# Performance work log

Measured on AMD Instinct MI355X. Metric: run time of the kernel, lower is better.

## Reference

```python
import jax, jax.numpy as jnp
import numpy as np

N_FREQS = 6  # PositionEmbedding default used by LISA


def setup_inputs() -> dict:
    key = jax.random.key(0)
    ks = jax.random.split(key, 8)
    B, L, N, D, H = 8, 32768, 2048, 64, 256
    in_dim = 1 * (2 * N_FREQS + 1) + 3 * D  # 13 + 192 = 205

    def w(k, i, o):
        return jax.random.normal(k, (i, o), jnp.float32) * (1.0 / np.sqrt(i))

    return {
        "coord": jax.random.uniform(ks[0], (B, L, 1), jnp.float32),
        "latent": jax.random.normal(ks[1], (B, N, D), jnp.float32),
        "W0": w(ks[2], in_dim, H), "b0": jnp.zeros((H,), jnp.float32),
        "W1": w(ks[3], H, H), "b1": jnp.zeros((H,), jnp.float32),
        "W2": w(ks[4], H, H), "b2": jnp.zeros((H,), jnp.float32),
        "W3": w(ks[5], H, H), "b3": jnp.zeros((H,), jnp.float32),
        "W4": w(ks[6], H, 1), "b4": jnp.zeros((1,), jnp.float32),
    }


def reference(coord, latent, W0, b0, W1, b1, W2, b2, W3, b3, W4, b4):
    B, N, D = latent.shape
    # feat_unfold: concat shifted-prev / self / shifted-next along channels
    feat = jnp.swapaxes(latent, 1, 2)                                   # [B, D, N]
    feat_prev = jnp.concatenate([feat[:, :, :1], feat[:, :, :-1]], axis=2)
    feat_next = jnp.concatenate([feat[:, :, 1:], feat[:, :, -1:]], axis=2)
    feat = jnp.concatenate([feat_prev, feat, feat_next], axis=1)        # [B, 3D, N]

    # grid_sample(bilinear, padding_mode='border', align_corners=False) on a
    # 1-row image: y coordinate 0 hits row 0 exactly, so only x interpolates.
    # torch mapping: ix = ((gx + 1) * W - 1) / 2 with gx = coord*2 - 1
    ix = coord[..., 0] * N - 0.5                                        # [B, L]
    x0 = jnp.floor(ix)
    t = ix - x0                                                         # lerp weight
    i0 = jnp.clip(x0.astype(jnp.int32), 0, N - 1)                       # border clamp
    i1 = jnp.clip(x0.astype(jnp.int32) + 1, 0, N - 1)
    f0 = jnp.take_along_axis(feat, i0[:, None, :], axis=2)              # [B, 3D, L]
    f1 = jnp.take_along_axis(feat, i1[:, None, :], axis=2)
    sampled = (1.0 - t)[:, None, :] * f0 + t[:, None, :] * f1
    sampled = jnp.swapaxes(sampled, 1, 2)                               # [B, L, 3D]

    # positional encoding: [x, sin(f x), cos(f x) for f in 1,2,4,8,16,32]
    freqs = 2.0 ** jnp.arange(N_FREQS, dtype=jnp.float32)
    ang = coord * freqs                                                 # [B, L, 6]
    pe = jnp.stack([jnp.sin(ang), jnp.cos(ang)], axis=-1)
    pe = pe.reshape(ang.shape[0], ang.shape[1], 2 * N_FREQS)            # [B, L, 12]

    inp = jnp.concatenate([coord, pe, sampled], axis=-1)                # [B, L, 205]

    h = jax.nn.relu(inp @ W0 + b0)
    h = jax.nn.relu(h @ W1 + b1)
    h = jax.nn.relu(h @ W2 + b2)
    h = jax.nn.relu(h @ W3 + b3)
    return h @ W4 + b4                                                  # [B, L, 1]
```

## Files before the change

kernel.cpp:

```cpp
#include <hip/hip_runtime.h>
#include <hip/hip_bf16.h>

typedef unsigned short ushort_t;
typedef unsigned int uint_t;
typedef __attribute__((ext_vector_type(8))) short short8;
typedef __attribute__((ext_vector_type(4))) float float4v;
typedef __attribute__((ext_vector_type(4))) uint_t uint4v;

#define NLAT 2048
#define DLAT 64

#define PW_BASE 128
#define PW0_OFF 0
#define PW1_OFF 57344
#define PW2_OFF 122880
#define PW3_OFF 188416

__device__ __forceinline__ float b2f(ushort_t u) {
  union { uint_t i; float f; } v; v.i = ((uint_t)u) << 16; return v.f;
}
__device__ __forceinline__ ushort_t f2b(float f) {
  uint_t x = __float_as_uint(f);
  uint_t r = (x + 0x7fffu + ((x >> 16) & 1u)) >> 16;
  return (ushort_t)r;
}
__device__ __forceinline__ uint_t pack2(float lo, float hi) {
  float2 t; t.x = lo; t.y = hi;
  union { __hip_bfloat162 h; uint_t u; } cv;
  cv.h = __float22bfloat162_rn(t);
  return cv.u;
}
__device__ __forceinline__ int imin(int a, int b) { return a < b ? a : b; }
__device__ __forceinline__ int imax(int a, int b) { return a > b ? a : b; }

__device__ __forceinline__ float ldv(const float* p, long i)    { return p[i]; }
__device__ __forceinline__ float ldv(const ushort_t* p, long i) { return b2f(p[i]); }
__device__ __forceinline__ void stv(float* p, long i, float v)    { p[i] = v; }
__device__ __forceinline__ void stv(ushort_t* p, long i, float v) { p[i] = f2b(v); }

__device__ __forceinline__ float4 load4f(const float* p) { return *(const float4*)p; }
__device__ __forceinline__ float4 load4f(const ushort_t* p) {
  uint2 u = *(const uint2*)p;
  float4 r;
  r.x = b2f((ushort_t)(u.x & 0xffffu)); r.y = b2f((ushort_t)(u.x >> 16));
  r.z = b2f((ushort_t)(u.y & 0xffffu)); r.w = b2f((ushort_t)(u.y >> 16));
  return r;
}

__device__ __forceinline__ void async_copy16(const ushort_t* g, ushort_t* l) {
  __builtin_amdgcn_global_load_lds(
      (const __attribute__((address_space(1))) void*)g,
      (__attribute__((address_space(3))) void*)l, 16, 0, 0);
}

__device__ __forceinline__ void stage_q(int gi, ushort_t* dst,
                                        const ushort_t* __restrict__ pw, int tid) {
  int layer = gi >> 2, q = gi & 3;
  int KT = (layer == 0) ? 7 : 8;
  int loff = (layer == 0) ? PW0_OFF : (layer == 1) ? PW1_OFF
           : (layer == 2) ? PW2_OFF : PW3_OFF;
  const ushort_t* src = pw + loff + q * KT * 2048;
  int n = KT * 256;
  for (int i = tid; i < n; i += 256)
    async_copy16(src + (size_t)i * 8, dst + (size_t)i * 8);
}

__global__ void detect_mode(const ushort_t* __restrict__ lat, int* __restrict__ flag) {
  if (threadIdx.x == 0) *flag = 0;
  __syncthreads();
  int big = 0;
  for (int i = threadIdx.x; i < 1024; i += 64) {
    float v = b2f(lat[i]);
    if (!(fabsf(v) < 1e5f)) big = 1;
  }
  if (__any(big) && threadIdx.x == 0) *flag = 1;
}

template <typename TI>
__global__ void pack_w_t(const TI* __restrict__ W0, const TI* __restrict__ W1,
                         const TI* __restrict__ W2, const TI* __restrict__ W3,
                         ushort_t* __restrict__ pw, const int* __restrict__ flag, int want)
{
  if (*flag != want) return;
  int g = blockIdx.x * blockDim.x + threadIdx.x;
  if (g >= 31 * 1024) return;
  int lane = g & 63, q = lane >> 4;
  int mt   = (g >> 6) & 15;
  int ktg  = g >> 10;
  const TI* W; ushort_t* dst; int kt, KT; bool isw0 = false;
  if (ktg < 7)       { W = W0; dst = pw + PW0_OFF; kt = ktg;      KT = 7; isw0 = true; }
  else if (ktg < 15) { W = W1; dst = pw + PW1_OFF; kt = ktg - 7;  KT = 8; }
  else if (ktg < 23) { W = W2; dst = pw + PW2_OFF; kt = ktg - 15; KT = 8; }
  else               { W = W3; dst = pw + PW3_OFF; kt = ktg - 23; KT = 8; }
  int col = mt * 16 + (lane & 15);
  uint_t words[4];
#pragma unroll
  for (int h = 0; h < 4; ++h) {
    ushort_t vv[2];
#pragma unroll
    for (int e = 0; e < 2; ++e) {
      int j = 2 * h + e;
      int f = 32 * kt + 16 * (j >> 2) + 4 * q + (j & 3);
      int row = f;
      if (isw0) row = (f < 192) ? (13 + f) : (f == 192 ? 0 : (f <= 204 ? f - 192 : -1));
      vv[e] = (row >= 0) ? f2b(ldv(W, (long)row * 256 + col)) : (ushort_t)0;
    }
    words[h] = (uint_t)vv[0] | ((uint_t)vv[1] << 16);
  }
  uint4 o; o.x = words[0]; o.y = words[1]; o.z = words[2]; o.w = words[3];
  *(uint4*)(dst + ((size_t)(mt * KT + kt) * 64 + lane) * 8) = o;
}

template <int KT>
__device__ __forceinline__ void run_layer(int base, float4v (&acc)[16][2],
                                          const uint4v (&hu)[8][2],
                                          ushort_t (*wbuf)[16384],
                                          const ushort_t* __restrict__ pw,
                                          int tid, int lane)
{
#pragma unroll
  for (int qq = 0; qq < 4; ++qq) {
    const int gi = base + qq;
    if (gi + 1 < 16) stage_q(gi + 1, wbuf[(gi + 1) & 1], pw, tid);
    const ushort_t* buf = wbuf[gi & 1];
#pragma unroll
    for (int m = 0; m < 4; ++m) {
      acc[qq * 4 + m][0] = (float4v){0.f, 0.f, 0.f, 0.f};
      acc[qq * 4 + m][1] = (float4v){0.f, 0.f, 0.f, 0.f};
    }
#pragma unroll
    for (int kt = 0; kt < KT; ++kt) {
      short8 b0 = __builtin_bit_cast(short8, hu[kt][0]);
      short8 b1 = __builtin_bit_cast(short8, hu[kt][1]);
#pragma unroll
      for (int m = 0; m < 4; ++m) {
        short8 a = *(const short8*)&buf[((size_t)(m * KT + kt) * 64 + lane) * 8];
        acc[qq * 4 + m][0] = __builtin_amdgcn_mfma_f32_16x16x32_bf16(a, b0, acc[qq * 4 + m][0], 0, 0, 0);
        acc[qq * 4 + m][1] = __builtin_amdgcn_mfma_f32_16x16x32_bf16(a, b1, acc[qq * 4 + m][1], 0, 0, 0);
      }
    }
    __syncthreads();
  }
}

__device__ __forceinline__ void convert_layer(float4v (&acc)[16][2], uint4v (&hu)[8][2],
                                              const float* bwl, int q)
{
#pragma unroll
  for (int mt = 0; mt < 16; ++mt) {
    float4 b4 = *(const float4*)&bwl[mt * 16 + 4 * q];
#pragma unroll
    for (int g = 0; g < 2; ++g) {
      float v0 = fmaxf(acc[mt][g][0] + b4.x, 0.f);
      float v1 = fmaxf(acc[mt][g][1] + b4.y, 0.f);
      float v2 = fmaxf(acc[mt][g][2] + b4.z, 0.f);
      float v3 = fmaxf(acc[mt][g][3] + b4.w, 0.f);
      hu[mt >> 1][g][(mt & 1) * 2 + 0] = pack2(v0, v1);
      hu[mt >> 1][g][(mt & 1) * 2 + 1] = pack2(v2, v3);
    }
  }
}

template <typename TI>
__global__ __launch_bounds__(256, 2) void lisa_fused_t(
    const TI* __restrict__ coord, const TI* __restrict__ latent,
    const TI* __restrict__ bias0, const TI* __restrict__ bias1,
    const TI* __restrict__ bias2, const TI* __restrict__ bias3,
    const TI* __restrict__ W4,    const TI* __restrict__ b4,
    const ushort_t* __restrict__ pw, TI* __restrict__ out,
    const int* __restrict__ flag, int want)
{
  if (*flag != want) return;
  __shared__ __align__(16) ushort_t wbuf[2][16384];
  __shared__ __align__(16) float bw[4 * 256 + 256 + 1];

  const int tid  = threadIdx.x;
  const int lane = tid & 63, q = lane >> 4, m15 = lane & 15;
  const int wv   = tid >> 6;
  const long pbase = (long)blockIdx.x * 128 + wv * 32 + m15;

  stage_q(0, wbuf[0], pw, tid);
  for (int i = tid; i < 1281; i += 256) {
    float v;
    if (i < 256)       v = ldv(bias0, i);
    else if (i < 512)  v = ldv(bias1, i - 256);
    else if (i < 768)  v = ldv(bias2, i - 512);
    else if (i < 1024) v = ldv(bias3, i - 768);
    else if (i < 1280) v = ldv(W4, i - 1024);
    else               v = ldv(b4, 0);
    bw[i] = v;
  }

  uint4v hu[8][2];
#pragma unroll
  for (int g = 0; g < 2; ++g) {
    long p = pbase + g * 16;
    float c   = ldv(coord, p);
    float ixv = c * 2048.0f - 0.5f;
    float x0f = floorf(ixv);
    float t   = ixv - x0f;
    int   x0  = (int)x0f;
    int   i0  = imin(imax(x0, 0), NLAT - 1);
    int   i1  = imin(imax(x0 + 1, 0), NLAT - 1);
    float w0 = 1.0f - t, w1 = t;
    int rows0[3] = { imax(i0 - 1, 0), i0, imin(i0 + 1, NLAT - 1) };
    int rows1[3] = { imax(i1 - 1, 0), i1, imin(i1 + 1, NLAT - 1) };
    const TI* lat = latent + (size_t)(p >> 15) * (NLAT * DLAT);
#pragma unroll
    for (int tb = 0; tb < 12; ++tb) {
      int region = tb >> 2;
      int d0 = 16 * (tb & 3) + 4 * q;
      float4 a = load4f(lat + (long)rows0[region] * DLAT + d0);
      float4 b = load4f(lat + (long)rows1[region] * DLAT + d0);
      hu[tb >> 1][g][(tb & 1) * 2 + 0] = pack2(w0 * a.x + w1 * b.x, w0 * a.y + w1 * b.y);
      hu[tb >> 1][g][(tb & 1) * 2 + 1] = pack2(w0 * a.z + w1 * b.z, w0 * a.w + w1 * b.w);
    }
    float pv[4];
#pragma unroll
    for (int s = 0; s < 4; ++s) {
      int f = 192 + 4 * q + s;
      float v = 0.0f;
      if (f == 192) v = c;
      else if (f <= 204) {
        int i = f - 193;
        float fr = (float)(1 << (i >> 1));
        float ang = c * fr;
        v = (i & 1) ? __cosf(ang) : __sinf(ang);
      }
      pv[s] = v;
    }
    hu[6][g][0] = pack2(pv[0], pv[1]);
    hu[6][g][1] = pack2(pv[2], pv[3]);
    hu[6][g][2] = 0; hu[6][g][3] = 0;
  }
  __syncthreads();

  float4v acc[16][2];

  run_layer<7>( 0, acc, hu, wbuf, pw, tid, lane);
  convert_layer(acc, hu, bw + 0 * 256, q);
  run_layer<8>( 4, acc, hu, wbuf, pw, tid, lane);
  convert_layer(acc, hu, bw + 1 * 256, q);
  run_layer<8>( 8, acc, hu, wbuf, pw, tid, lane);
  convert_layer(acc, hu, bw + 2 * 256, q);
  run_layer<8>(12, acc, hu, wbuf, pw, tid, lane);

  float partial0 = 0.f, partial1 = 0.f;
#pragma unroll
  for (int mt = 0; mt < 16; ++mt) {
    float4 b3v = *(const float4*)&bw[3 * 256 + mt * 16 + 4 * q];
    float4 w4v = *(const float4*)&bw[1024 + mt * 16 + 4 * q];
    float v;
    v = fmaxf(acc[mt][0][0] + b3v.x, 0.f); partial0 += v * w4v.x;
    v = fmaxf(acc[mt][0][1] + b3v.y, 0.f); partial0 += v * w4v.y;
    v = fmaxf(acc[mt][0][2] + b3v.z, 0.f); partial0 += v * w4v.z;
    v = fmaxf(acc[mt][0][3] + b3v.w, 0.f); partial0 += v * w4v.w;
    v = fmaxf(acc[mt][1][0] + b3v.x, 0.f); partial1 += v * w4v.x;
    v = fmaxf(acc[mt][1][1] + b3v.y, 0.f); partial1 += v * w4v.y;
    v = fmaxf(acc[mt][1][2] + b3v.z, 0.f); partial1 += v * w4v.z;
    v = fmaxf(acc[mt][1][3] + b3v.w, 0.f); partial1 += v * w4v.w;
  }
  partial0 += __shfl_xor(partial0, 16, 64);
  partial0 += __shfl_xor(partial0, 32, 64);
  partial1 += __shfl_xor(partial1, 16, 64);
  partial1 += __shfl_xor(partial1, 32, 64);
  if (lane < 16) {
    float bb = bw[1280];
    stv(out, pbase,      partial0 + bb);
    stv(out, pbase + 16, partial1 + bb);
  }
}

extern "C" void kernel_launch(void* const* d_in, const int* in_sizes, int n_in,
                              void* d_out, int out_size, void* d_ws, size_t ws_size,
                              hipStream_t stream) {
  int* flag = (int*)d_ws;
  ushort_t* pw = (ushort_t*)d_ws + PW_BASE;

  detect_mode<<<1, 64, 0, stream>>>((const ushort_t*)d_in[1], flag);

  pack_w_t<float><<<62, 512, 0, stream>>>(
      (const float*)d_in[2], (const float*)d_in[4], (const float*)d_in[6],
      (const float*)d_in[8], pw, flag, 1);
  lisa_fused_t<float><<<2048, 256, 0, stream>>>(
      (const float*)d_in[0], (const float*)d_in[1],
      (const float*)d_in[3], (const float*)d_in[5], (const float*)d_in[7],
      (const float*)d_in[9], (const float*)d_in[10], (const float*)d_in[11],
      pw, (float*)d_out, flag, 1);

  pack_w_t<ushort_t><<<62, 512, 0, stream>>>(
      (const ushort_t*)d_in[2], (const ushort_t*)d_in[4], (const ushort_t*)d_in[6],
      (const ushort_t*)d_in[8], pw, flag, 0);
  lisa_fused_t<ushort_t><<<2048, 256, 0, stream>>>(
      (const ushort_t*)d_in[0], (const ushort_t*)d_in[1],
      (const ushort_t*)d_in[3], (const ushort_t*)d_in[5], (const ushort_t*)d_in[7],
      (const ushort_t*)d_in[9], (const ushort_t*)d_in[10], (const ushort_t*)d_in[11],
      pw, (ushort_t*)d_out, flag, 0);
}
```

Measured before the change: 236.7 us.

## Switch MLP matmuls from 16x16x32 to 32x32x16 MFMA with repacked weights

Replaces the 16x16x32 bf16 MFMA tiling with 32x32x16 MFMA, so each wave handles 32 points as one B operand. The packed weight layout, K-row permutation for the activation handoff, embedding/gather layout and final reduction are all rewritten to match. The aim is fewer MFMA instructions and LDS reads per FLOP, and a lookahead load of the A fragment to overlap LDS reads with MFMA. It risks higher register pressure from the 16-float accumulators and depends on the new K-permutation being correct.

```diff
diff --git a/kernel.cpp b/kernel.cpp
--- a/kernel.cpp
+++ b/kernel.cpp
@@ -5,6 +5,7 @@
 typedef unsigned int uint_t;
 typedef __attribute__((ext_vector_type(8))) short short8;
 typedef __attribute__((ext_vector_type(4))) float float4v;
+typedef __attribute__((ext_vector_type(16))) float float16v;
 typedef __attribute__((ext_vector_type(4))) uint_t uint4v;
 
 #define NLAT 2048
@@ -12,9 +13,9 @@
 
 #define PW_BASE 128
 #define PW0_OFF 0
-#define PW1_OFF 57344
-#define PW2_OFF 122880
-#define PW3_OFF 188416
+#define PW1_OFF 53248
+#define PW2_OFF 118784
+#define PW3_OFF 184320
 
 __device__ __forceinline__ float b2f(ushort_t u) {
   union { uint_t i; float f; } v; v.i = ((uint_t)u) << 16; return v.f;
@@ -53,14 +54,15 @@
       (__attribute__((address_space(3))) void*)l, 16, 0, 0);
 }
 
-__device__ __forceinline__ void stage_q(int gi, ushort_t* dst,
-                                        const ushort_t* __restrict__ pw, int tid) {
-  int layer = gi >> 2, q = gi & 3;
-  int KT = (layer == 0) ? 7 : 8;
-  int loff = (layer == 0) ? PW0_OFF : (layer == 1) ? PW1_OFF
-           : (layer == 2) ? PW2_OFF : PW3_OFF;
-  const ushort_t* src = pw + loff + q * KT * 2048;
-  int n = KT * 256;
+__device__ __forceinline__ void stage_gi(int gi, ushort_t* dst,
+                                         const ushort_t* __restrict__ pw, int tid) {
+  int layer = gi >> 2, qq = gi & 3;
+  const ushort_t* src; int n;
+  if (layer == 0) { src = pw + PW0_OFF + (size_t)qq * 13312; n = 1664; }
+  else {
+    int loff = (layer == 1) ? PW1_OFF : (layer == 2) ? PW2_OFF : PW3_OFF;
+    src = pw + loff + (size_t)qq * 16384; n = 2048;
+  }
   for (int i = tid; i < n; i += 256)
     async_copy16(src + (size_t)i * 8, dst + (size_t)i * 8);
 }
@@ -83,80 +85,91 @@
 {
   if (*flag != want) return;
   int g = blockIdx.x * blockDim.x + threadIdx.x;
-  if (g >= 31 * 1024) return;
-  int lane = g & 63, q = lane >> 4;
-  int mt   = (g >> 6) & 15;
-  int ktg  = g >> 10;
-  const TI* W; ushort_t* dst; int kt, KT; bool isw0 = false;
-  if (ktg < 7)       { W = W0; dst = pw + PW0_OFF; kt = ktg;      KT = 7; isw0 = true; }
-  else if (ktg < 15) { W = W1; dst = pw + PW1_OFF; kt = ktg - 7;  KT = 8; }
-  else if (ktg < 23) { W = W2; dst = pw + PW2_OFF; kt = ktg - 15; KT = 8; }
-  else               { W = W3; dst = pw + PW3_OFF; kt = ktg - 23; KT = 8; }
-  int col = mt * 16 + (lane & 15);
+  if (g >= 488 * 64) return;
+  int lane = g & 63, h = lane >> 5;
+  int fid  = g >> 6;
+  const TI* W; ushort_t* dst; int mt, kt, KTL, layer;
+  if (fid < 104) { layer = 0; W = W0; dst = pw + PW0_OFF; mt = fid / 13; kt = fid % 13; KTL = 13; }
+  else {
+    int f2 = fid - 104;
+    layer = 1 + f2 / 128;
+    int r = f2 & 127; mt = r >> 4; kt = r & 15; KTL = 16;
+    W = (layer == 1) ? W1 : (layer == 2) ? W2 : W3;
+    dst = pw + ((layer == 1) ? PW1_OFF : (layer == 2) ? PW2_OFF : PW3_OFF);
+  }
+  int col = mt * 32 + (lane & 31);
   uint_t words[4];
 #pragma unroll
-  for (int h = 0; h < 4; ++h) {
+  for (int hw = 0; hw < 4; ++hw) {
     ushort_t vv[2];
 #pragma unroll
     for (int e = 0; e < 2; ++e) {
-      int j = 2 * h + e;
-      int f = 32 * kt + 16 * (j >> 2) + 4 * q + (j & 3);
-      int row = f;
-      if (isw0) row = (f < 192) ? (13 + f) : (f == 192 ? 0 : (f <= 204 ? f - 192 : -1));
+      int j = 2 * hw + e;
+      int k = 16 * kt + 8 * h + j;
+      int row;
+      if (layer == 0) {
+        row = (k < 192) ? (13 + k) : (k == 192 ? 0 : (k <= 204 ? k - 192 : -1));
+      } else {
+        int blk = k >> 5, kl = k & 31;
+        int t = (kl >> 4) & 1, h2 = (kl >> 3) & 1, u = (kl >> 2) & 1, b = kl & 3;
+        row = 32 * blk + 8 * (2 * t + u) + 4 * h2 + b;
+      }
       vv[e] = (row >= 0) ? f2b(ldv(W, (long)row * 256 + col)) : (ushort_t)0;
     }
-    words[h] = (uint_t)vv[0] | ((uint_t)vv[1] << 16);
+    words[hw] = (uint_t)vv[0] | ((uint_t)vv[1] << 16);
   }
   uint4 o; o.x = words[0]; o.y = words[1]; o.z = words[2]; o.w = words[3];
-  *(uint4*)(dst + ((size_t)(mt * KT + kt) * 64 + lane) * 8) = o;
-}
-
-template <int KT>
-__device__ __forceinline__ void run_layer(int base, float4v (&acc)[16][2],
-                                          const uint4v (&hu)[8][2],
+  *(uint4*)(dst + ((size_t)(mt * KTL + kt) * 64 + lane) * 8) = o;
+}
+
+template <int KT, int BASE>
+__device__ __forceinline__ void run_layer(float16v (&acc)[8],
+                                          const uint4v (&hu)[16],
                                           ushort_t (*wbuf)[16384],
                                           const ushort_t* __restrict__ pw,
                                           int tid, int lane)
 {
 #pragma unroll
   for (int qq = 0; qq < 4; ++qq) {
-    const int gi = base + qq;
-    if (gi + 1 < 16) stage_q(gi + 1, wbuf[(gi + 1) & 1], pw, tid);
+    constexpr int KTC = KT;
+    const int gi = BASE + qq;
+    if (gi + 1 < 16) stage_gi(gi + 1, wbuf[(gi + 1) & 1], pw, tid);
     const ushort_t* buf = wbuf[gi & 1];
-#pragma unroll
-    for (int m = 0; m < 4; ++m) {
-      acc[qq * 4 + m][0] = (float4v){0.f, 0.f, 0.f, 0.f};
-      acc[qq * 4 + m][1] = (float4v){0.f, 0.f, 0.f, 0.f};
-    }
-#pragma unroll
-    for (int kt = 0; kt < KT; ++kt) {
-      short8 b0 = __builtin_bit_cast(short8, hu[kt][0]);
-      short8 b1 = __builtin_bit_cast(short8, hu[kt][1]);
-#pragma unroll
-      for (int m = 0; m < 4; ++m) {
-        short8 a = *(const short8*)&buf[((size_t)(m * KT + kt) * 64 + lane) * 8];
-        acc[qq * 4 + m][0] = __builtin_amdgcn_mfma_f32_16x16x32_bf16(a, b0, acc[qq * 4 + m][0], 0, 0, 0);
-        acc[qq * 4 + m][1] = __builtin_amdgcn_mfma_f32_16x16x32_bf16(a, b1, acc[qq * 4 + m][1], 0, 0, 0);
+    float16v c0, c1;
+#pragma unroll
+    for (int i = 0; i < 16; ++i) { c0[i] = 0.f; c1[i] = 0.f; }
+    short8 aL, aH;
+    aL = *(const short8*)&buf[((size_t)(0 * KTC + 0) * 64 + lane) * 8];
+#pragma unroll
+    for (int kt = 0; kt < KTC; ++kt) {
+      aH = *(const short8*)&buf[((size_t)(1 * KTC + kt) * 64 + lane) * 8];
+      short8 b = __builtin_bit_cast(short8, hu[kt]);
+      c0 = __builtin_amdgcn_mfma_f32_32x32x16_bf16(aL, b, c0, 0, 0, 0);
+      if (kt + 1 < KTC)
+        aL = *(const short8*)&buf[((size_t)(0 * KTC + kt + 1) * 64 + lane) * 8];
+      c1 = __builtin_amdgcn_mfma_f32_32x32x16_bf16(aH, b, c1, 0, 0, 0);
+    }
+    acc[2 * qq]     = c0;
+    acc[2 * qq + 1] = c1;
+    __syncthreads();
+  }
+}
+
+__device__ __forceinline__ void convert_layer(float16v (&acc)[8], uint4v (&hu)[16],
+                                              const float* bwl, int h)
+{
+#pragma unroll
+  for (int mt = 0; mt < 8; ++mt) {
+#pragma unroll
+    for (int a = 0; a < 4; ++a) {
+      float4 bv = *(const float4*)&bwl[32 * mt + 8 * a + 4 * h];
+#pragma unroll
+      for (int b2 = 0; b2 < 2; ++b2) {
+        int rr = 4 * a + 2 * b2;
+        float v0 = fmaxf(acc[mt][rr]     + ((const float*)&bv)[2 * b2],     0.f);
+        float v1 = fmaxf(acc[mt][rr + 1] + ((const float*)&bv)[2 * b2 + 1], 0.f);
+        hu[2 * mt + (rr >> 3)][(rr & 7) >> 1] = pack2(v0, v1);
       }
-    }
-    __syncthreads();
-  }
-}
-
-__device__ __forceinline__ void convert_layer(float4v (&acc)[16][2], uint4v (&hu)[8][2],
-                                              const float* bwl, int q)
-{
-#pragma unroll
-  for (int mt = 0; mt < 16; ++mt) {
-    float4 b4 = *(const float4*)&bwl[mt * 16 + 4 * q];
-#pragma unroll
-    for (int g = 0; g < 2; ++g) {
-      float v0 = fmaxf(acc[mt][g][0] + b4.x, 0.f);
-      float v1 = fmaxf(acc[mt][g][1] + b4.y, 0.f);
-      float v2 = fmaxf(acc[mt][g][2] + b4.z, 0.f);
-      float v3 = fmaxf(acc[mt][g][3] + b4.w, 0.f);
-      hu[mt >> 1][g][(mt & 1) * 2 + 0] = pack2(v0, v1);
-      hu[mt >> 1][g][(mt & 1) * 2 + 1] = pack2(v2, v3);
     }
   }
 }
@@ -175,11 +188,11 @@
   __shared__ __align__(16) float bw[4 * 256 + 256 + 1];
 
   const int tid  = threadIdx.x;
-  const int lane = tid & 63, q = lane >> 4, m15 = lane & 15;
+  const int lane = tid & 63, h = lane >> 5, n32 = lane & 31;
   const int wv   = tid >> 6;
-  const long pbase = (long)blockIdx.x * 128 + wv * 32 + m15;
-
-  stage_q(0, wbuf[0], pw, tid);
+  const long p   = (long)blockIdx.x * 128 + wv * 32 + n32;
+
+  stage_gi(0, wbuf[0], pw, tid);
   for (int i = tid; i < 1281; i += 256) {
     float v;
     if (i < 256)       v = ldv(bias0, i);
@@ -191,10 +204,8 @@
     bw[i] = v;
   }
 
-  uint4v hu[8][2];
-#pragma unroll
-  for (int g = 0; g < 2; ++g) {
-    long p = pbase + g * 16;
+  uint4v hu[16];
+  {
     float c   = ldv(coord, p);
     float ixv = c * 2048.0f - 0.5f;
     float x0f = floorf(ixv);
@@ -207,18 +218,22 @@
     int rows1[3] = { imax(i1 - 1, 0), i1, imin(i1 + 1, NLAT - 1) };
     const TI* lat = latent + (size_t)(p >> 15) * (NLAT * DLAT);
 #pragma unroll
-    for (int tb = 0; tb < 12; ++tb) {
-      int region = tb >> 2;
-      int d0 = 16 * (tb & 3) + 4 * q;
-      float4 a = load4f(lat + (long)rows0[region] * DLAT + d0);
-      float4 b = load4f(lat + (long)rows1[region] * DLAT + d0);
-      hu[tb >> 1][g][(tb & 1) * 2 + 0] = pack2(w0 * a.x + w1 * b.x, w0 * a.y + w1 * b.y);
-      hu[tb >> 1][g][(tb & 1) * 2 + 1] = pack2(w0 * a.z + w1 * b.z, w0 * a.w + w1 * b.w);
-    }
-    float pv[4];
-#pragma unroll
-    for (int s = 0; s < 4; ++s) {
-      int f = 192 + 4 * q + s;
+    for (int kt = 0; kt < 12; ++kt) {
+      int f0 = 16 * kt + 8 * h;
+      int region = f0 >> 6, d0 = f0 & 63;
+      float4 a0 = load4f(lat + (long)rows0[region] * DLAT + d0);
+      float4 a1 = load4f(lat + (long)rows0[region] * DLAT + d0 + 4);
+      float4 b0 = load4f(lat + (long)rows1[region] * DLAT + d0);
+      float4 b1 = load4f(lat + (long)rows1[region] * DLAT + d0 + 4);
+      hu[kt][0] = pack2(w0 * a0.x + w1 * b0.x, w0 * a0.y + w1 * b0.y);
+      hu[kt][1] = pack2(w0 * a0.z + w1 * b0.z, w0 * a0.w + w1 * b0.w);
+      hu[kt][2] = pack2(w0 * a1.x + w1 * b1.x, w0 * a1.y + w1 * b1.y);
+      hu[kt][3] = pack2(w0 * a1.z + w1 * b1.z, w0 * a1.w + w1 * b1.w);
+    }
+    float e[8];
+#pragma unroll
+    for (int j = 0; j < 8; ++j) {
+      int f = 192 + 8 * h + j;
       float v = 0.0f;
       if (f == 192) v = c;
       else if (f <= 204) {
@@ -227,48 +242,42 @@
         float ang = c * fr;
         v = (i & 1) ? __cosf(ang) : __sinf(ang);
       }
-      pv[s] = v;
-    }
-    hu[6][g][0] = pack2(pv[0], pv[1]);
-    hu[6][g][1] = pack2(pv[2], pv[3]);
-    hu[6][g][2] = 0; hu[6][g][3] = 0;
+      e[j] = v;
+    }
+    hu[12][0] = pack2(e[0], e[1]);
+    hu[12][1] = pack2(e[2], e[3]);
+    hu[12][2] = pack2(e[4], e[5]);
+    hu[12][3] = pack2(e[6], e[7]);
   }
   __syncthreads();
 
-  float4v acc[16][2];
-
-  run_layer<7>( 0, acc, hu, wbuf, pw, tid, lane);
-  convert_layer(acc, hu, bw + 0 * 256, q);
-  run_layer<8>( 4, acc, hu, wbuf, pw, tid, lane);
-  convert_layer(acc, hu, bw + 1 * 256, q);
-  run_layer<8>( 8, acc, hu, wbuf, pw, tid, lane);
-  convert_layer(acc, hu, bw + 2 * 256, q);
-  run_layer<8>(12, acc, hu, wbuf, pw, tid, lane);
-
-  float partial0 = 0.f, partial1 = 0.f;
-#pragma unroll
-  for (int mt = 0; mt < 16; ++mt) {
-    float4 b3v = *(const float4*)&bw[3 * 256 + mt * 16 + 4 * q];
-    float4 w4v = *(const float4*)&bw[1024 + mt * 16 + 4 * q];
-    float v;
-    v = fmaxf(acc[mt][0][0] + b3v.x, 0.f); partial0 += v * w4v.x;
-    v = fmaxf(acc[mt][0][1] + b3v.y, 0.f); partial0 += v * w4v.y;
-    v = fmaxf(acc[mt][0][2] + b3v.z, 0.f); partial0 += v * w4v.z;
-    v = fmaxf(acc[mt][0][3] + b3v.w, 0.f); partial0 += v * w4v.w;
-    v = fmaxf(acc[mt][1][0] + b3v.x, 0.f); partial1 += v * w4v.x;
-    v = fmaxf(acc[mt][1][1] + b3v.y, 0.f); partial1 += v * w4v.y;
-    v = fmaxf(acc[mt][1][2] + b3v.z, 0.f); partial1 += v * w4v.z;
-    v = fmaxf(acc[mt][1][3] + b3v.w, 0.f); partial1 += v * w4v.w;
-  }
-  partial0 += __shfl_xor(partial0, 16, 64);
-  partial0 += __shfl_xor(partial0, 32, 64);
-  partial1 += __shfl_xor(partial1, 16, 64);
-  partial1 += __shfl_xor(partial1, 32, 64);
-  if (lane < 16) {
-    float bb = bw[1280];
-    stv(out, pbase,      partial0 + bb);
-    stv(out, pbase + 16, partial1 + bb);
-  }
+  float16v acc[8];
+
+  run_layer<13,  0>(acc, hu, wbuf, pw, tid, lane);
+  convert_layer(acc, hu, bw + 0 * 256, h);
+  run_layer<16,  4>(acc, hu, wbuf, pw, tid, lane);
+  convert_layer(acc, hu, bw + 1 * 256, h);
+  run_layer<16,  8>(acc, hu, wbuf, pw, tid, lane);
+  convert_layer(acc, hu, bw + 2 * 256, h);
+  run_layer<16, 12>(acc, hu, wbuf, pw, tid, lane);
+
+  float partial = 0.f;
+#pragma unroll
+  for (int mt = 0; mt < 8; ++mt) {
+#pragma unroll
+    for (int a = 0; a < 4; ++a) {
+      float4 b3v = *(const float4*)&bw[3 * 256 + 32 * mt + 8 * a + 4 * h];
+      float4 w4v = *(const float4*)&bw[1024 + 32 * mt + 8 * a + 4 * h];
+#pragma unroll
+      for (int e = 0; e < 4; ++e) {
+        int rr = 4 * a + e;
+        float v = fmaxf(acc[mt][rr] + ((const float*)&b3v)[e], 0.f);
+        partial += v * ((const float*)&w4v)[e];
+      }
+    }
+  }
+  partial += __shfl_xor(partial, 32, 64);
+  if (lane < 32) stv(out, p, partial + bw[1280]);
 }
 
 extern "C" void kernel_launch(void* const* d_in, const int* in_sizes, int n_in,
@@ -279,7 +288,7 @@
 
   detect_mode<<<1, 64, 0, stream>>>((const ushort_t*)d_in[1], flag);
 
-  pack_w_t<float><<<62, 512, 0, stream>>>(
+  pack_w_t<float><<<61, 512, 0, stream>>>(
       (const float*)d_in[2], (const float*)d_in[4], (const float*)d_in[6],
       (const float*)d_in[8], pw, flag, 1);
   lisa_fused_t<float><<<2048, 256, 0, stream>>>(
@@ -288,7 +297,7 @@
       (const float*)d_in[9], (const float*)d_in[10], (const float*)d_in[11],
       pw, (float*)d_out, flag, 1);
 
-  pack_w_t<ushort_t><<<62, 512, 0, stream>>>(
+  pack_w_t<ushort_t><<<61, 512, 0, stream>>>(
       (const ushort_t*)d_in[2], (const ushort_t*)d_in[4], (const ushort_t*)d_in[6],
       (const ushort_t*)d_in[8], pw, flag, 0);
   lisa_fused_t<ushort_t><<<2048, 256, 0, stream>>>(
```

New measurement: 264.9 us. +11.9%, slower.
